# Performance work log

Measured on AMD Instinct MI355X. Metric: run time of the kernel, lower is better.

## Reference

```python
import jax, jax.numpy as jnp
import numpy as np

HEADS = 8
MAX_REL = 256
D_MODEL = 512
FFN_DIM = 2048
LN_EPS = 1e-3  # keras LayerNormalization default
NEG_INF = -1e9


def _layer_norm(x, gamma, beta):
    mu = jnp.mean(x, axis=-1, keepdims=True)
    var = jnp.var(x, axis=-1, keepdims=True)
    return (x - mu) * jax.lax.rsqrt(var + LN_EPS) * gamma + beta


def _mhra(q_in, k_in, v_in, mask, p):
    """Multi-head relative-position (Shaw-style) attention.
    mask: (B, Lq, Lk), 1.0 = masked position (added as -1e9).
    """
    B, Lq, D = q_in.shape
    Lk = k_in.shape[1]
    H = HEADS
    depth = D // H
    q = (q_in @ p['Wq'] + p['bq']).reshape(B, Lq, H, depth).transpose(0, 2, 1, 3)
    k = (k_in @ p['Wk'] + p['bk']).reshape(B, Lk, H, depth).transpose(0, 2, 1, 3)
    v = (v_in @ p['Wv'] + p['bv']).reshape(B, Lk, H, depth).transpose(0, 2, 1, 3)
    # content logits (B,H,Lq,Lk)
    logits = jnp.einsum('bhqd,bhkd->bhqk', q, k)
    # relative-position logits: project q onto clipped relative embeddings
    rel_q = jnp.einsum('bhqd,rd->bhqr', q, p['rel_emb'])  # (B,H,Lq,2K+1)
    rel_idx = jnp.clip(jnp.arange(Lk)[None, :] - jnp.arange(Lq)[:, None],
                       -MAX_REL, MAX_REL) + MAX_REL  # (Lq,Lk)
    rel_logits = jnp.take_along_axis(
        rel_q, jnp.broadcast_to(rel_idx[None, None], (B, H, Lq, Lk)), axis=-1)
    scores = (logits + rel_logits) / jnp.sqrt(jnp.asarray(depth, q.dtype))
    scores = scores + mask[:, None, :, :] * NEG_INF
    weights = jax.nn.softmax(scores, axis=-1)
    out = jnp.einsum('bhqk,bhkd->bhqd', weights, v)
    out = out.transpose(0, 2, 1, 3).reshape(B, Lq, D)
    out = out @ p['Wo'] + p['bo']
    return out, weights


def _make_attn_params(key, prefix):
    ks = jax.random.split(key, 5)
    s = 0.02
    return {
        prefix + 'Wq': jax.random.normal(ks[0], (D_MODEL, D_MODEL), jnp.float32) * s,
        prefix + 'bq': jnp.zeros((D_MODEL,), jnp.float32),
        prefix + 'Wk': jax.random.normal(ks[1], (D_MODEL, D_MODEL), jnp.float32) * s,
        prefix + 'bk': jnp.zeros((D_MODEL,), jnp.float32),
        prefix + 'Wv': jax.random.normal(ks[2], (D_MODEL, D_MODEL), jnp.float32) * s,
        prefix + 'bv': jnp.zeros((D_MODEL,), jnp.float32),
        prefix + 'Wo': jax.random.normal(ks[3], (D_MODEL, D_MODEL), jnp.float32) * s,
        prefix + 'bo': jnp.zeros((D_MODEL,), jnp.float32),
        prefix + 'rel_emb': jax.random.normal(ks[4], (2 * MAX_REL + 1, D_MODEL // HEADS), jnp.float32) * s,
        prefix + 'ln_g': jnp.ones((D_MODEL,), jnp.float32),
        prefix + 'ln_b': jnp.zeros((D_MODEL,), jnp.float32),
    }


def setup_inputs() -> dict:
    key = jax.random.key(0)
    ks = jax.random.split(key, 8)
    B, Lq, Lk = 8, 1024, 1024
    inputs = jax.random.normal(ks[0], (B, Lq, D_MODEL), jnp.float32)
    enc_kv = jax.random.normal(ks[1], (B, Lk, D_MODEL), jnp.float32)
    padding_mask = jnp.zeros((B, Lq, Lk), jnp.float32)  # no encoder padding
    causal = (jnp.arange(Lk)[None, :] > jnp.arange(Lq)[:, None]).astype(jnp.float32)
    lookahead_mask = jnp.broadcast_to(causal[None], (B, Lq, Lq)).astype(jnp.float32)
    d = {'inputs': inputs, 'enc_kv': enc_kv,
         'padding_mask': padding_mask, 'lookahead_mask': lookahead_mask,
         'training': 0}
    d.update(_make_attn_params(ks[2], 'sa_'))
    d.update(_make_attn_params(ks[3], 'ca_'))
    s = 0.02
    d['ffn_W1'] = jax.random.normal(ks[4], (D_MODEL, FFN_DIM), jnp.float32) * s
    d['ffn_b1'] = jnp.zeros((FFN_DIM,), jnp.float32)
    d['ffn_W2'] = jax.random.normal(ks[5], (FFN_DIM, D_MODEL), jnp.float32) * s
    d['ffn_b2'] = jnp.zeros((D_MODEL,), jnp.float32)
    d['ffn_ln_g'] = jnp.ones((D_MODEL,), jnp.float32)
    d['ffn_ln_b'] = jnp.zeros((D_MODEL,), jnp.float32)
    return d


def reference(inputs, enc_kv, padding_mask, lookahead_mask, training,
              sa_Wq, sa_bq, sa_Wk, sa_bk, sa_Wv, sa_bv, sa_Wo, sa_bo,
              sa_rel_emb, sa_ln_g, sa_ln_b,
              ca_Wq, ca_bq, ca_Wk, ca_bk, ca_Wv, ca_bv, ca_Wo, ca_bo,
              ca_rel_emb, ca_ln_g, ca_ln_b,
              ffn_W1, ffn_b1, ffn_W2, ffn_b2, ffn_ln_g, ffn_ln_b):
    sa = {'Wq': sa_Wq, 'bq': sa_bq, 'Wk': sa_Wk, 'bk': sa_bk,
          'Wv': sa_Wv, 'bv': sa_bv, 'Wo': sa_Wo, 'bo': sa_bo,
          'rel_emb': sa_rel_emb}
    ca = {'Wq': ca_Wq, 'bq': ca_bq, 'Wk': ca_Wk, 'bk': ca_bk,
          'Wv': ca_Wv, 'bv': ca_bv, 'Wo': ca_Wo, 'bo': ca_bo,
          'rel_emb': ca_rel_emb}
    # self attention + residual + norm (dropout identity at inference)
    attn_out, attn_w = _mhra(inputs, inputs, inputs, lookahead_mask, sa)
    attn_out = _layer_norm(inputs + attn_out, sa_ln_g, sa_ln_b)
    # cross attention + residual + norm
    ca_out, ca_w = _mhra(attn_out, enc_kv, enc_kv, padding_mask, ca)
    ca_out = _layer_norm(attn_out + ca_out, ca_ln_g, ca_ln_b)
    # pointwise FFN + residual + norm
    h = jax.nn.relu(ca_out @ ffn_W1 + ffn_b1) @ ffn_W2 + ffn_b2
    out = _layer_norm(h + ca_out, ffn_ln_g, ffn_ln_b)
    return out, attn_w, ca_w
```

## Files before the change

### kernel.cpp

```cpp
#include <hip/hip_runtime.h>
#include <hip/hip_bf16.h>
#include <cstdio>


typedef __attribute__((ext_vector_type(8))) short short8v;
typedef __attribute__((ext_vector_type(4))) short short4v;
typedef __attribute__((ext_vector_type(4))) float f32x4;

static __device__ __forceinline__ unsigned short f2bf(float f) {
    unsigned int u = __float_as_uint(f);
    unsigned int r = (u + 0x7fffu + ((u >> 16) & 1u)) >> 16;
    return (unsigned short)r;
}
static __device__ __forceinline__ float bf2f(unsigned short s) {
    return __uint_as_float(((unsigned int)s) << 16);
}

static __device__ __forceinline__ f32x4 mfma_bf16(short8v a, short8v b, f32x4 c) {
    return __builtin_amdgcn_mfma_f32_16x16x32_bf16(a, b, c, 0, 0, 0);
}

static __device__ __forceinline__ void async16(const void* g, void* l) {
    __builtin_amdgcn_global_load_lds(
        (const __attribute__((address_space(1))) unsigned int*)g,
        (__attribute__((address_space(3))) unsigned int*)l,
        16, 0, 0);
}

static __device__ __forceinline__ int swz8(int bid, int nwg) {
    return (bid & 7) * (nwg >> 3) + (bid >> 3);
}


static __device__ __forceinline__ void gemm_core(
    unsigned short* As, unsigned short* Bs,
    const unsigned short* __restrict__ A, int lda,
    const unsigned short* __restrict__ BT, int ldb,
    const float* __restrict__ bias, float* __restrict__ Cf,
    unsigned short* __restrict__ Cb, int ldc,
    int m0, int n0, int Kblk, int relu)
{
    const int t = threadIdx.x, lane = t & 63, w = t >> 6;
    const int wm = w >> 1, wn = w & 1;
    f32x4 acc[4][4];
#pragma unroll
    for (int m = 0; m < 4; ++m)
#pragma unroll
        for (int n = 0; n < 4; ++n) acc[m][n] = (f32x4){0.f, 0.f, 0.f, 0.f};

    const int srow = lane >> 2;
    const int sgl  = (lane & 3) ^ ((lane >> 3) & 3);
    for (int k0 = 0; k0 < Kblk; k0 += 32) {
#pragma unroll
        for (int c = w; c < 8; c += 4) {
            async16(A  + (size_t)(m0 + c * 16 + srow) * lda + k0 + sgl * 8, As + c * 512);
            async16(BT + (size_t)(n0 + c * 16 + srow) * ldb + k0 + sgl * 8, Bs + c * 512);
        }
        __syncthreads();
        short8v a[4], b[4];
        const int g = lane >> 4, l15 = lane & 15;
        const int ss = (g ^ ((l15 >> 1) & 3)) * 8;
#pragma unroll
        for (int m = 0; m < 4; ++m)
            a[m] = *(const short8v*)&As[(wm * 64 + m * 16 + l15) * 32 + ss];
#pragma unroll
        for (int n = 0; n < 4; ++n)
            b[n] = *(const short8v*)&Bs[(wn * 64 + n * 16 + l15) * 32 + ss];
#pragma unroll
        for (int m = 0; m < 4; ++m)
#pragma unroll
            for (int n = 0; n < 4; ++n)
                acc[m][n] = mfma_bf16(a[m], b[n], acc[m][n]);
        __syncthreads();
    }
#pragma unroll
    for (int m = 0; m < 4; ++m) {
        int gm = m0 + wm * 64 + m * 16 + (lane >> 4) * 4;
#pragma unroll
        for (int n = 0; n < 4; ++n) {
            int gn = n0 + wn * 64 + n * 16 + (lane & 15);
            float bv = bias ? bias[gn] : 0.f;
#pragma unroll
            for (int j = 0; j < 4; ++j) {
                float v = acc[m][n][j] + bv;
                if (relu) v = fmaxf(v, 0.f);
                size_t off = (size_t)(gm + j) * ldc + gn;
                if (Cf) Cf[off] = v;
                if (Cb) Cb[off] = f2bf(v);
            }
        }
    }
}

__global__ __launch_bounds__(256) void gemm_std(
    const unsigned short* __restrict__ A, int lda,
    const unsigned short* __restrict__ BT, int ldb,
    const float* __restrict__ bias,
    float* __restrict__ Cf, unsigned short* __restrict__ Cb,
    int N, int Kblk, int relu)
{
    __shared__ __attribute__((aligned(16))) unsigned short As[128 * 32];
    __shared__ __attribute__((aligned(16))) unsigned short Bs[128 * 32];
    const int kz = blockIdx.z;
    const int nwg = gridDim.x * gridDim.y;
    const int s = swz8(blockIdx.x + gridDim.x * blockIdx.y, nwg);
    const int bx = s % gridDim.x, by = s / gridDim.x;
    const size_t part = (size_t)kz * gridDim.y * 128 * N;
    gemm_core(As, Bs, A + kz * Kblk, lda, BT + kz * Kblk, ldb,
              kz == 0 ? bias : nullptr,
              Cf ? Cf + part : nullptr, Cb, N,
              by * 128, bx * 128, Kblk, relu);
}

__global__ __launch_bounds__(256) void gemm_ca(
    const unsigned short* __restrict__ Ekv, const unsigned short* __restrict__ Xq,
    const unsigned short* __restrict__ WkvT, const unsigned short* __restrict__ WqT,
    const float* __restrict__ bkv, const float* __restrict__ bq,
    unsigned short* __restrict__ KV, unsigned short* __restrict__ Q)
{
    __shared__ __attribute__((aligned(16))) unsigned short As[128 * 32];
    __shared__ __attribute__((aligned(16))) unsigned short Bs[128 * 32];
    const int nwg = gridDim.x * gridDim.y;
    const int s = swz8(blockIdx.x + gridDim.x * blockIdx.y, nwg);
    const int bx = s % gridDim.x, by = s / gridDim.x;
    if (bx < 8)
        gemm_core(As, Bs, Ekv, 512, WkvT, 512, bkv, nullptr, KV, 1024,
                  by * 128, bx * 128, 512, 0);
    else
        gemm_core(As, Bs, Xq, 512, WqT, 512, bq, nullptr, Q, 512,
                  by * 128, (bx - 8) * 128, 512, 0);
}

__global__ __launch_bounds__(256, 3) void fused_attn(
    const unsigned short* __restrict__ Qp, int qstride,
    const unsigned short* __restrict__ Kp, int kstride,
    const unsigned short* __restrict__ Vt,
    const unsigned short* __restrict__ relW,
    const unsigned short* __restrict__ maskb,
    float* __restrict__ Wout,
    unsigned short* __restrict__ Hout)
{
    __shared__ __attribute__((aligned(16))) unsigned short Qs[16 * 64];
    __shared__ __attribute__((aligned(16))) unsigned short U[24576];
    __shared__ float Red[2][4][16];
    unsigned short* Ks  = U;
    unsigned short* Rel = U;
    unsigned short* Pl  = U;
    unsigned short* Vs  = U + 16384;
    const int t = threadIdx.x, lane = t & 63, w = t >> 6;
    const int g = lane >> 4, l15 = lane & 15;
    const int s = swz8(blockIdx.x + gridDim.x * blockIdx.y, 4096);
    const int bh = s >> 6, b = bh >> 3, h = bh & 7;
    const int q0 = (s & 63) * 16;
    const int sgl8 = (lane & 7) ^ ((lane >> 3) & 7);

    if (w < 2) {
        int row = w * 8 + (lane >> 3);
        async16(Qp + (size_t)(b * 1024 + q0 + row) * qstride + h * 64 + sgl8 * 8,
                &Qs[w * 512]);
    }
    __syncthreads();

    short8v qa[2];
#pragma unroll
    for (int kk = 0; kk < 2; ++kk)
        qa[kk] = *(const short8v*)&Qs[l15 * 64 + (((kk * 4 + g) ^ (l15 & 7))) * 8];

    f32x4 acc[16];
#pragma unroll
    for (int i = 0; i < 16; ++i) acc[i] = (f32x4){0.f, 0.f, 0.f, 0.f};

#pragma unroll
    for (int qtr = 0; qtr < 4; ++qtr) {
#pragma unroll
        for (int c = 0; c < 8; ++c) {
            int rbase = w * 64 + c * 8;
            async16(Kp + (size_t)(b * 1024 + qtr * 256 + rbase + (lane >> 3)) * kstride
                       + h * 64 + sgl8 * 8,
                    &Ks[rbase * 64]);
        }
        __syncthreads();
#pragma unroll
        for (int n = 0; n < 4; ++n) {
            int row = w * 64 + n * 16 + l15;
            short8v kb0 = *(const short8v*)&Ks[row * 64 + ((g ^ (row & 7))) * 8];
            short8v kb1 = *(const short8v*)&Ks[row * 64 + (((4 + g) ^ (row & 7))) * 8];
            acc[qtr * 4 + n] = mfma_bf16(qa[0], kb0, acc[qtr * 4 + n]);
            acc[qtr * 4 + n] = mfma_bf16(qa[1], kb1, acc[qtr * 4 + n]);
        }
        __syncthreads();
    }

    for (int rs = w; rs < 33; rs += 4) {
        int rc = rs * 16 + l15;
        int re = rc > 512 ? 512 : rc;
        short8v b0 = *(const short8v*)(relW + (size_t)re * 64 + g * 8);
        short8v b1 = *(const short8v*)(relW + (size_t)re * 64 + 32 + g * 8);
        f32x4 r4 = (f32x4){0.f, 0.f, 0.f, 0.f};
        r4 = mfma_bf16(qa[0], b0, r4);
        r4 = mfma_bf16(qa[1], b1, r4);
#pragma unroll
        for (int j = 0; j < 4; ++j)
            Rel[(g * 4 + j) * 528 + rs * 16 + l15] = f2bf(r4[j]);
    }
    __syncthreads();

    const int qb = q0 + g * 4;
    const int ql = g * 4;
    const unsigned short* mrow = maskb + ((size_t)b * 1024 + qb) * 1024;
#pragma unroll
    for (int na = 0; na < 16; ++na) {
        int k = (na >> 2) * 256 + w * 64 + (na & 3) * 16 + l15;
#pragma unroll
        for (int j = 0; j < 4; ++j) {
            int q = qb + j;
            int d = k - q; d = d < -256 ? -256 : (d > 256 ? 256 : d);
            float rel = bf2f(Rel[(ql + j) * 528 + d + 256]);
            float mv = bf2f(mrow[(size_t)j * 1024 + k]);
            acc[na][j] = (acc[na][j] + rel) * 0.125f + mv;
        }
    }

    float mx[4];
#pragma unroll
    for (int j = 0; j < 4; ++j) {
        float m = acc[0][j];
#pragma unroll
        for (int na = 1; na < 16; ++na) m = fmaxf(m, acc[na][j]);
#pragma unroll
        for (int off = 1; off < 16; off <<= 1) m = fmaxf(m, __shfl_xor(m, off));
        mx[j] = m;
    }
    if (l15 == 0) {
#pragma unroll
        for (int j = 0; j < 4; ++j) Red[0][w][ql + j] = mx[j];
    }
    __syncthreads();
#pragma unroll
    for (int j = 0; j < 4; ++j) {
        float m = Red[0][0][ql + j];
        m = fmaxf(m, Red[0][1][ql + j]);
        m = fmaxf(m, Red[0][2][ql + j]);
        m = fmaxf(m, Red[0][3][ql + j]);
        mx[j] = m;
    }

    float sm[4] = {0.f, 0.f, 0.f, 0.f};
#pragma unroll
    for (int na = 0; na < 16; ++na)
#pragma unroll
        for (int j = 0; j < 4; ++j) {
            float e = __expf(acc[na][j] - mx[j]);
            acc[na][j] = e;
            sm[j] += e;
        }
#pragma unroll
    for (int j = 0; j < 4; ++j)
#pragma unroll
        for (int off = 1; off < 16; off <<= 1) sm[j] += __shfl_xor(sm[j], off);
    if (l15 == 0) {
#pragma unroll
        for (int j = 0; j < 4; ++j) Red[1][w][ql + j] = sm[j];
    }
    __syncthreads();
#pragma unroll
    for (int j = 0; j < 4; ++j) {
        float ssum = Red[1][0][ql + j] + Red[1][1][ql + j]
                   + Red[1][2][ql + j] + Red[1][3][ql + j];
        sm[j] = 1.0f / ssum;
    }

    float* wbase = Wout + ((size_t)bh * 1024 + qb) * 1024;
#pragma unroll
    for (int na = 0; na < 16; ++na) {
        int k = (na >> 2) * 256 + w * 64 + (na & 3) * 16 + l15;
#pragma unroll
        for (int j = 0; j < 4; ++j) {
            float p = acc[na][j] * sm[j];
            wbase[(size_t)j * 1024 + k] = p;
            Pl[((k >> 3) * 16 + (ql + j)) * 8 + (k & 7)] = f2bf(p);
        }
    }
    __syncthreads();

    f32x4 oacc = (f32x4){0.f, 0.f, 0.f, 0.f};
#pragma unroll
    for (int c = 0; c < 8; ++c) {
        {
            int idx = w * 4;
#pragma unroll
            for (int i = 0; i < 4; ++i) {
                int d = (idx + i) * 4 + (lane >> 4);
                int gl = (lane & 15) ^ (d & 15);
                async16(Vt + ((size_t)bh * 64 + d) * 1024 + c * 128 + gl * 8,
                        &Vs[(idx + i) * 512]);
            }
        }
        __syncthreads();
#pragma unroll
        for (int ks = 0; ks < 4; ++ks) {
            int kg = c * 4 + ks;
            short8v a = *(const short8v*)&Pl[((kg * 4 + g) * 16 + l15) * 8];
            int rowv = w * 16 + l15;
            short8v bb = *(const short8v*)&Vs[rowv * 128 + (((ks * 4 + g) ^ (rowv & 15))) * 8];
            oacc = mfma_bf16(a, bb, oacc);
        }
        __syncthreads();
    }
#pragma unroll
    for (int j = 0; j < 4; ++j)
        Hout[(size_t)(b * 1024 + q0 + g * 4 + j) * 512 + h * 64 + w * 16 + l15]
            = f2bf(oacc[j]);
}

__global__ __launch_bounds__(256) void transpose_v(
    const unsigned short* __restrict__ Vb, int stride, unsigned short* __restrict__ Vt)
{
    __shared__ unsigned short T[128][72];
    const int bh = blockIdx.y, b = bh >> 3, h = bh & 7;
    const int k0 = blockIdx.x * 128;
    const int t = threadIdx.x;
    {
        int r = t >> 1, half = t & 1;
        const unsigned short* gp = Vb + (size_t)(b * 1024 + k0 + r) * stride + h * 64 + half * 32;
#pragma unroll
        for (int i = 0; i < 8; ++i)
            *(short4v*)&T[r][half * 32 + i * 4] = *(const short4v*)(gp + i * 4);
    }
    __syncthreads();
    {
        int d = t >> 2, qtr = t & 3;
        unsigned short* gp = Vt + ((size_t)bh * 64 + d) * 1024 + k0 + qtr * 32;
#pragma unroll
        for (int i = 0; i < 32; i += 4) {
            short4v v;
            v.x = T[qtr * 32 + i + 0][d];
            v.y = T[qtr * 32 + i + 1][d];
            v.z = T[qtr * 32 + i + 2][d];
            v.w = T[qtr * 32 + i + 3][d];
            *(short4v*)(gp + i) = v;
        }
    }
}

__global__ __launch_bounds__(128) void ln512(
    const float* __restrict__ Xp0, const float* __restrict__ Xp1,
    const float* __restrict__ Res,
    const float* __restrict__ g, const float* __restrict__ be,
    float* __restrict__ out, unsigned short* __restrict__ outb)
{
    const size_t row = blockIdx.x;
    const int t = threadIdx.x;
    float4 x = *(const float4*)(Xp0 + row * 512 + t * 4);
    float4 r = *(const float4*)(Res + row * 512 + t * 4);
    x.x += r.x; x.y += r.y; x.z += r.z; x.w += r.w;
    if (Xp1) {
        float4 p = *(const float4*)(Xp1 + row * 512 + t * 4);
        x.x += p.x; x.y += p.y; x.z += p.z; x.w += p.w;
    }
    float s  = x.x + x.y + x.z + x.w;
    float ss = x.x * x.x + x.y * x.y + x.z * x.z + x.w * x.w;
#pragma unroll
    for (int o = 32; o > 0; o >>= 1) { s += __shfl_xor(s, o); ss += __shfl_xor(ss, o); }
    __shared__ float sm[2], sq[2];
    if ((t & 63) == 0) { sm[t >> 6] = s; sq[t >> 6] = ss; }
    __syncthreads();
    s = sm[0] + sm[1]; ss = sq[0] + sq[1];
    const float mean = s * (1.f / 512.f);
    const float var  = ss * (1.f / 512.f) - mean * mean;
    const float rstd = rsqrtf(var + 1e-3f);
    float4 gv = *(const float4*)(g + t * 4), bv = *(const float4*)(be + t * 4);
    float4 o;
    o.x = (x.x - mean) * rstd * gv.x + bv.x;
    o.y = (x.y - mean) * rstd * gv.y + bv.y;
    o.z = (x.z - mean) * rstd * gv.z + bv.z;
    o.w = (x.w - mean) * rstd * gv.w + bv.w;
    *(float4*)(out + row * 512 + t * 4) = o;
    if (outb) {
        short4v q4;
        q4.x = f2bf(o.x); q4.y = f2bf(o.y); q4.z = f2bf(o.z); q4.w = f2bf(o.w);
        *(short4v*)(outb + row * 512 + t * 4) = q4;
    }
}

static __device__ __forceinline__ void wt_tile(
    const float* __restrict__ W, unsigned short* __restrict__ WT,
    int K, int N, int k0, int n0)
{
    __shared__ float T[64][68];
    const int t = threadIdx.x;
    int r = t >> 4, c = (t & 15) * 4;
#pragma unroll
    for (int p = 0; p < 4; ++p) {
        float4 v = *(const float4*)(W + (size_t)(k0 + r + p * 16) * N + n0 + c);
        T[r + p * 16][c + 0] = v.x; T[r + p * 16][c + 1] = v.y;
        T[r + p * 16][c + 2] = v.z; T[r + p * 16][c + 3] = v.w;
    }
    __syncthreads();
#pragma unroll
    for (int p = 0; p < 4; ++p) {
        int n = r + p * 16;
        short4v o;
        o.x = f2bf(T[c + 0][n]); o.y = f2bf(T[c + 1][n]);
        o.z = f2bf(T[c + 2][n]); o.w = f2bf(T[c + 3][n]);
        *(short4v*)(WT + (size_t)(n0 + n) * K + k0 + c) = o;
    }
}

__global__ __launch_bounds__(256) void wt_cast(
    const float* __restrict__ W, unsigned short* __restrict__ WT, int K, int N)
{
    wt_tile(W, WT, K, N, blockIdx.y * 64, blockIdx.x * 64);
}

struct Ptr8 {
    const float* s[8];
    unsigned short* d[8];
};

__global__ __launch_bounds__(256) void wt_cast8(Ptr8 p)
{
    wt_tile(p.s[blockIdx.z], p.d[blockIdx.z], 512, 512,
            blockIdx.y * 64, blockIdx.x * 64);
}

__global__ __launch_bounds__(256) void misc_prep(
    const float* __restrict__ sarel, const float* __restrict__ carel,
    unsigned short* __restrict__ relSA, unsigned short* __restrict__ relCA,
    const float* __restrict__ sabq, const float* __restrict__ sabk,
    const float* __restrict__ sabv, float* __restrict__ bqkv,
    const float* __restrict__ cabk, const float* __restrict__ cabv,
    float* __restrict__ bkv)
{
    const int bid = blockIdx.x, t = threadIdx.x;
    if (bid < 33) {
        int i = bid * 256 + t;
        if (i < 8208) {
            float4 v = *(const float4*)(sarel + (size_t)i * 4);
            short4v s;
            s.x = f2bf(v.x); s.y = f2bf(v.y); s.z = f2bf(v.z); s.w = f2bf(v.w);
            *(short4v*)(relSA + (size_t)i * 4) = s;
        }
    } else if (bid < 66) {
        int i = (bid - 33) * 256 + t;
        if (i < 8208) {
            float4 v = *(const float4*)(carel + (size_t)i * 4);
            short4v s;
            s.x = f2bf(v.x); s.y = f2bf(v.y); s.z = f2bf(v.z); s.w = f2bf(v.w);
            *(short4v*)(relCA + (size_t)i * 4) = s;
        }
    } else if (bid == 66) {
        for (int i = t; i < 1536; i += 256)
            bqkv[i] = i < 512 ? sabq[i] : (i < 1024 ? sabk[i - 512] : sabv[i - 1024]);
    } else {
        for (int i = t; i < 1024; i += 256)
            bkv[i] = i < 512 ? cabk[i] : cabv[i - 512];
    }
}

__global__ __launch_bounds__(256) void cast_all(
    const float* __restrict__ a, unsigned short* __restrict__ oa,
    const float* __restrict__ b, unsigned short* __restrict__ ob,
    const float* __restrict__ m0, unsigned short* __restrict__ om0,
    const float* __restrict__ m1, unsigned short* __restrict__ om1)
{
    size_t i = (size_t)blockIdx.x * 256 + threadIdx.x;
    const float* src; unsigned short* dst; float scale;
    if (i < 1048576)      { src = a;  dst = oa;  scale = 1.f; }
    else if (i < 2097152) { src = b;  dst = ob;  scale = 1.f; i -= 1048576; }
    else if (i < 4194304) { src = m0; dst = om0; scale = -1e9f; i -= 2097152; }
    else                  { src = m1; dst = om1; scale = -1e9f; i -= 4194304; }
    float4 v = *(const float4*)(src + i * 4);
    short4v s;
    s.x = f2bf(v.x * scale); s.y = f2bf(v.y * scale);
    s.z = f2bf(v.z * scale); s.w = f2bf(v.w * scale);
    *(short4v*)(dst + i * 4) = s;
}


extern "C" void kernel_launch(void* const* d_in, const int* in_sizes, int n_in,
                              void* d_out, int out_size, void* d_ws, size_t ws_size,
                              hipStream_t stream)
{
    (void)in_sizes; (void)n_in; (void)out_size;
    const float* inputs    = (const float*)d_in[0];
    const float* enc_kv    = (const float*)d_in[1];
    const float* pad_mask  = (const float*)d_in[2];
    const float* look_mask = (const float*)d_in[3];
    const float* saWq  = (const float*)d_in[5];
    const float* sabq  = (const float*)d_in[6];
    const float* saWk  = (const float*)d_in[7];
    const float* sabk  = (const float*)d_in[8];
    const float* saWv  = (const float*)d_in[9];
    const float* sabv  = (const float*)d_in[10];
    const float* saWo  = (const float*)d_in[11];
    const float* sabo  = (const float*)d_in[12];
    const float* sarel = (const float*)d_in[13];
    const float* salg  = (const float*)d_in[14];
    const float* salb  = (const float*)d_in[15];
    const float* caWq  = (const float*)d_in[16];
    const float* cabq  = (const float*)d_in[17];
    const float* caWk  = (const float*)d_in[18];
    const float* cabk  = (const float*)d_in[19];
    const float* caWv  = (const float*)d_in[20];
    const float* cabv  = (const float*)d_in[21];
    const float* caWo  = (const float*)d_in[22];
    const float* cabo  = (const float*)d_in[23];
    const float* carel = (const float*)d_in[24];
    const float* calg  = (const float*)d_in[25];
    const float* calb  = (const float*)d_in[26];
    const float* fW1   = (const float*)d_in[27];
    const float* fb1   = (const float*)d_in[28];
    const float* fW2   = (const float*)d_in[29];
    const float* fb2   = (const float*)d_in[30];
    const float* flg   = (const float*)d_in[31];
    const float* flb   = (const float*)d_in[32];

    float* out    = (float*)d_out;
    float* attn_w = out + (size_t)8 * 1024 * 512;
    float* ca_w   = attn_w + (size_t)8 * 8 * 1024 * 1024;

    char* ws = (char*)d_ws;
    size_t off = 0;
    unsigned short* WTa = (unsigned short*)(ws + off); off += 8519936;
    float* bqkv = (float*)(ws + off); off += 8192;
    float* bkv  = (float*)(ws + off); off += 8192;
    unsigned short* Abf   = (unsigned short*)(ws + off); off += 8388608;
    unsigned short* Ebf   = (unsigned short*)(ws + off); off += 8388608;
    unsigned short* x1bf  = (unsigned short*)(ws + off); off += 8388608;
    unsigned short* Qca   = (unsigned short*)(ws + off); off += 8388608;
    unsigned short* heads = (unsigned short*)(ws + off); off += 8388608;
    unsigned short* Vt    = (unsigned short*)(ws + off); off += 8388608;
    unsigned short* mskSA = (unsigned short*)(ws + off); off += 16777216;
    unsigned short* mskCA = (unsigned short*)(ws + off); off += 16777216;
    unsigned short* KV    = (unsigned short*)(ws + off); off += 16777216;
    unsigned short* big   = (unsigned short*)(ws + off); off += 33554432;
    float* x1 = (float*)(ws + off); off += 16777216;
    float* x2 = (float*)(ws + off); off += 16777216;
    float* Pb = (float*)(ws + off); off += 33554432;
    if (ws_size < off) {
        fprintf(stderr, "kernel_launch: ws too small (%zu < %zu)\n", ws_size, off);
        return;
    }
    float* Pb1 = Pb + 4194304;
    unsigned short* QKV    = big;
    unsigned short* hidden = big;
    unsigned short* x2bf   = Abf;

    unsigned short* saWqT = WTa + 0;
    unsigned short* saWkT = WTa + 262144;
    unsigned short* saWvT = WTa + 524288;
    unsigned short* saWoT = WTa + 786432;
    unsigned short* caWqT = WTa + 1048576;
    unsigned short* caWkT = WTa + 1310720;
    unsigned short* caWvT = WTa + 1572864;
    unsigned short* caWoT = WTa + 1835008;
    unsigned short* W1T   = WTa + 2097152;
    unsigned short* W2T   = WTa + 3145728;
    unsigned short* relSA = WTa + 4194304;
    unsigned short* relCA = WTa + 4227136;

    const dim3 T256(256), T128(128);

    Ptr8 p8;
    p8.s[0] = saWq; p8.d[0] = saWqT;
    p8.s[1] = saWk; p8.d[1] = saWkT;
    p8.s[2] = saWv; p8.d[2] = saWvT;
    p8.s[3] = saWo; p8.d[3] = saWoT;
    p8.s[4] = caWq; p8.d[4] = caWqT;
    p8.s[5] = caWk; p8.d[5] = caWkT;
    p8.s[6] = caWv; p8.d[6] = caWvT;
    p8.s[7] = caWo; p8.d[7] = caWoT;
    wt_cast8<<<dim3(8, 8, 8), T256, 0, stream>>>(p8);
    wt_cast<<<dim3(32, 8), T256, 0, stream>>>(fW1, W1T, 512, 2048);
    wt_cast<<<dim3(8, 32), T256, 0, stream>>>(fW2, W2T, 2048, 512);
    misc_prep<<<dim3(68), T256, 0, stream>>>(sarel, carel, relSA, relCA,
                                             sabq, sabk, sabv, bqkv, cabk, cabv, bkv);
    cast_all<<<dim3(24576), T256, 0, stream>>>(inputs, Abf, enc_kv, Ebf,
                                               look_mask, mskSA, pad_mask, mskCA);

    gemm_std<<<dim3(12, 64, 1), T256, 0, stream>>>(Abf, 512, WTa, 512, bqkv,
                                                   nullptr, QKV, 1536, 512, 0);
    transpose_v<<<dim3(8, 64), T256, 0, stream>>>(QKV + 1024, 1536, Vt);
    fused_attn<<<dim3(64, 64), T256, 0, stream>>>(QKV, 1536, QKV + 512, 1536, Vt,
                                                  relSA, mskSA, attn_w, heads);
    gemm_std<<<dim3(4, 64, 2), T256, 0, stream>>>(heads, 512, saWoT, 512, sabo,
                                                  Pb, nullptr, 512, 256, 0);
    ln512<<<dim3(8192), T128, 0, stream>>>(Pb, Pb1, inputs, salg, salb, x1, x1bf);

    gemm_ca<<<dim3(12, 64), T256, 0, stream>>>(Ebf, x1bf, caWkT, caWqT,
                                               bkv, cabq, KV, Qca);
    transpose_v<<<dim3(8, 64), T256, 0, stream>>>(KV + 512, 1024, Vt);
    fused_attn<<<dim3(64, 64), T256, 0, stream>>>(Qca, 512, KV, 1024, Vt,
                                                  relCA, mskCA, ca_w, heads);
    gemm_std<<<dim3(4, 64, 2), T256, 0, stream>>>(heads, 512, caWoT, 512, cabo,
                                                  Pb, nullptr, 512, 256, 0);
    ln512<<<dim3(8192), T128, 0, stream>>>(Pb, Pb1, x1, calg, calb, x2, x2bf);

    gemm_std<<<dim3(16, 64, 1), T256, 0, stream>>>(x2bf, 512, W1T, 512, fb1,
                                                   nullptr, hidden, 2048, 512, 1);
    gemm_std<<<dim3(4, 64, 2), T256, 0, stream>>>(hidden, 2048, W2T, 2048, fb2,
                                                  Pb, nullptr, 512, 1024, 0);
    ln512<<<dim3(8192), T128, 0, stream>>>(Pb, Pb1, x2, flg, flb, out, nullptr);
}
```

Measured before the change: 520.3 us.

## Double GEMM K-step to 64 with 8-way XOR swizzle; add nontemporal stores/loads

The shared GEMM core now stages a 64-wide K slice per iteration instead of 32, with a new 8-way XOR swizzle for the LDS tiles. This halves the number of barrier pairs and doubles the MFMA work between syncs. LDS use per GEMM block doubles to 32 KB, which may reduce occupancy. The attention kernel also writes the large fp32 weight output with nontemporal stores, and the cast kernel reads its inputs with nontemporal loads, both to reduce cache pollution.

```diff
diff --git a/kernel.cpp b/kernel.cpp
--- a/kernel.cpp
+++ b/kernel.cpp
@@ -42,35 +42,43 @@
 {
     const int t = threadIdx.x, lane = t & 63, w = t >> 6;
     const int wm = w >> 1, wn = w & 1;
+    const int g = lane >> 4, l15 = lane & 15;
     f32x4 acc[4][4];
 #pragma unroll
     for (int m = 0; m < 4; ++m)
 #pragma unroll
         for (int n = 0; n < 4; ++n) acc[m][n] = (f32x4){0.f, 0.f, 0.f, 0.f};
 
-    const int srow = lane >> 2;
-    const int sgl  = (lane & 3) ^ ((lane >> 3) & 3);
-    for (int k0 = 0; k0 < Kblk; k0 += 32) {
-#pragma unroll
-        for (int c = w; c < 8; c += 4) {
-            async16(A  + (size_t)(m0 + c * 16 + srow) * lda + k0 + sgl * 8, As + c * 512);
-            async16(BT + (size_t)(n0 + c * 16 + srow) * ldb + k0 + sgl * 8, Bs + c * 512);
+    const int sgl8 = (lane & 7) ^ ((lane >> 3) & 7);
+    for (int k0 = 0; k0 < Kblk; k0 += 64) {
+#pragma unroll
+        for (int i = 0; i < 4; ++i) {
+            int rbase = w * 32 + i * 8;
+            async16(A  + (size_t)(m0 + rbase + (lane >> 3)) * lda + k0 + sgl8 * 8,
+                    As + rbase * 64);
+            async16(BT + (size_t)(n0 + rbase + (lane >> 3)) * ldb + k0 + sgl8 * 8,
+                    Bs + rbase * 64);
         }
         __syncthreads();
-        short8v a[4], b[4];
-        const int g = lane >> 4, l15 = lane & 15;
-        const int ss = (g ^ ((l15 >> 1) & 3)) * 8;
-#pragma unroll
-        for (int m = 0; m < 4; ++m)
-            a[m] = *(const short8v*)&As[(wm * 64 + m * 16 + l15) * 32 + ss];
-#pragma unroll
-        for (int n = 0; n < 4; ++n)
-            b[n] = *(const short8v*)&Bs[(wn * 64 + n * 16 + l15) * 32 + ss];
-#pragma unroll
-        for (int m = 0; m < 4; ++m)
-#pragma unroll
-            for (int n = 0; n < 4; ++n)
-                acc[m][n] = mfma_bf16(a[m], b[n], acc[m][n]);
+#pragma unroll
+        for (int kk = 0; kk < 2; ++kk) {
+            short8v a[4], b[4];
+#pragma unroll
+            for (int m = 0; m < 4; ++m) {
+                int row = wm * 64 + m * 16 + l15;
+                a[m] = *(const short8v*)&As[row * 64 + (((kk * 4 + g) ^ (row & 7))) * 8];
+            }
+#pragma unroll
+            for (int n = 0; n < 4; ++n) {
+                int row = wn * 64 + n * 16 + l15;
+                b[n] = *(const short8v*)&Bs[row * 64 + (((kk * 4 + g) ^ (row & 7))) * 8];
+            }
+#pragma unroll
+            for (int m = 0; m < 4; ++m)
+#pragma unroll
+                for (int n = 0; n < 4; ++n)
+                    acc[m][n] = mfma_bf16(a[m], b[n], acc[m][n]);
+        }
         __syncthreads();
     }
 #pragma unroll
@@ -99,8 +107,8 @@
     float* __restrict__ Cf, unsigned short* __restrict__ Cb,
     int N, int Kblk, int relu)
 {
-    __shared__ __attribute__((aligned(16))) unsigned short As[128 * 32];
-    __shared__ __attribute__((aligned(16))) unsigned short Bs[128 * 32];
+    __shared__ __attribute__((aligned(16))) unsigned short As[128 * 64];
+    __shared__ __attribute__((aligned(16))) unsigned short Bs[128 * 64];
     const int kz = blockIdx.z;
     const int nwg = gridDim.x * gridDim.y;
     const int s = swz8(blockIdx.x + gridDim.x * blockIdx.y, nwg);
@@ -118,8 +126,8 @@
     const float* __restrict__ bkv, const float* __restrict__ bq,
     unsigned short* __restrict__ KV, unsigned short* __restrict__ Q)
 {
-    __shared__ __attribute__((aligned(16))) unsigned short As[128 * 32];
-    __shared__ __attribute__((aligned(16))) unsigned short Bs[128 * 32];
+    __shared__ __attribute__((aligned(16))) unsigned short As[128 * 64];
+    __shared__ __attribute__((aligned(16))) unsigned short Bs[128 * 64];
     const int nwg = gridDim.x * gridDim.y;
     const int s = swz8(blockIdx.x + gridDim.x * blockIdx.y, nwg);
     const int bx = s % gridDim.x, by = s / gridDim.x;
@@ -277,7 +285,7 @@
 #pragma unroll
         for (int j = 0; j < 4; ++j) {
             float p = acc[na][j] * sm[j];
-            wbase[(size_t)j * 1024 + k] = p;
+            __builtin_nontemporal_store(p, &wbase[(size_t)j * 1024 + k]);
             Pl[((k >> 3) * 16 + (ql + j)) * 8 + (k & 7)] = f2bf(p);
         }
     }
@@ -470,7 +478,12 @@
     else if (i < 2097152) { src = b;  dst = ob;  scale = 1.f; i -= 1048576; }
     else if (i < 4194304) { src = m0; dst = om0; scale = -1e9f; i -= 2097152; }
     else                  { src = m1; dst = om1; scale = -1e9f; i -= 4194304; }
-    float4 v = *(const float4*)(src + i * 4);
+    const float4* sp = (const float4*)(src + i * 4);
+    float4 v;
+    v.x = __builtin_nontemporal_load(&((const float*)sp)[0]);
+    v.y = __builtin_nontemporal_load(&((const float*)sp)[1]);
+    v.z = __builtin_nontemporal_load(&((const float*)sp)[2]);
+    v.w = __builtin_nontemporal_load(&((const float*)sp)[3]);
     short4v s;
     s.x = f2bf(v.x * scale); s.y = f2bf(v.y * scale);
     s.z = f2bf(v.z * scale); s.w = f2bf(v.w * scale);
```

New measurement: 494.1 us. 5.0% less time.
